# Performance work log

Hardware: AMD Instinct MI355X
Metric: run time of the kernel (lower is better)

Reference implementation:

```python
import jax, jax.numpy as jnp
import numpy as np


def _gru(x, h0, Wi, Wh, bi, bh):
    """PyTorch-equations GRU. x: (T,B,D), Wi: (3H,D), Wh: (3H,H). Returns (ys, hT)."""
    xW = jnp.einsum('tbd,gd->tbg', x, Wi) + bi  # (T,B,3H) precomputed input proj
    def step(h, xw):
        hw = h @ Wh.T + bh
        xr, xz, xn = jnp.split(xw, 3, axis=-1)
        hr, hz, hn = jnp.split(hw, 3, axis=-1)
        r = jax.nn.sigmoid(xr + hr)
        z = jax.nn.sigmoid(xz + hz)
        n = jnp.tanh(xn + r * hn)
        h_new = (1.0 - z) * n + z * h
        return h_new, h_new
    hT, ys = jax.lax.scan(step, h0, xW)
    return ys, hT


def _bigru(x, WiF, WhF, biF, bhF, WiB, WhB, biB, bhB):
    B = x.shape[1]
    H = WhF.shape[1]
    h0 = jnp.zeros((B, H), x.dtype)
    yf, hf = _gru(x, h0, WiF, WhF, biF, bhF)
    yb, hb = _gru(x[::-1], h0, WiB, WhB, biB, bhB)
    return jnp.concatenate([yf, yb[::-1]], axis=-1), jnp.stack([hf, hb], axis=0)


def _ln(x, g, b, eps=1e-5):
    mu = x.mean(-1, keepdims=True)
    var = ((x - mu) ** 2).mean(-1, keepdims=True)
    return (x - mu) * jax.lax.rsqrt(var + eps) * g + b


def _forward(tokens, emb,
             s_WiF, s_WhF, s_biF, s_bhF, s_lnF_g, s_lnF_b,
             s_Wi_f, s_Wh_f, s_bi_f, s_bh_f, s_Wi_b, s_Wh_b, s_bi_b, s_bh_b,
             s_ln_g, s_ln_b, s_linW, s_linb,
             d_WiF, d_WhF, d_biF, d_bhF, d_lnF_g, d_lnF_b,
             d_Wi_f, d_Wh_f, d_bi_f, d_bh_f, d_Wi_b, d_Wh_b, d_bi_b, d_bh_b,
             d_ln_g, d_ln_b, out_W, out_b):
    S, T, B = tokens.shape
    H = s_WhF.shape[1]
    # sentence loop is batch-independent -> fold sentences into batch
    x = emb[tokens]                                  # (S,T,B,E)
    x = x.transpose(1, 0, 2, 3).reshape(T, S * B, -1)  # (T, S*B, E)
    h0 = jnp.zeros((S * B, H), x.dtype)
    y, _ = _gru(x, h0, s_WiF, s_WhF, s_biF, s_bhF)
    y = _ln(y, s_lnF_g, s_lnF_b)
    y, _ = _bigru(y, s_Wi_f, s_Wh_f, s_bi_f, s_bh_f, s_Wi_b, s_Wh_b, s_bi_b, s_bh_b)
    y = _ln(y, s_ln_g, s_ln_b)
    y = jnp.tanh(y @ s_linW.T + s_linb)              # (T, S*B, H)
    store = y.mean(axis=0).reshape(S, B, H)          # per-sentence mean-pooled cell
    # document-level encoder over sentence sequence
    h0d = jnp.zeros((B, H), x.dtype)
    y, _ = _gru(store, h0d, d_WiF, d_WhF, d_biF, d_bhF)
    y = _ln(y, d_lnF_g, d_lnF_b)
    y, _ = _bigru(y, d_Wi_f, d_Wh_f, d_bi_f, d_bh_f, d_Wi_b, d_Wh_b, d_bi_b, d_bh_b)
    y = _ln(y, d_ln_g, d_ln_b)
    return jax.nn.sigmoid(y @ out_W.T + out_b)       # (S, B, O)


def setup_inputs() -> dict:
    V, E, H, O = 32000, 256, 256, 2
    S, T, B = 96, 32, 32
    keys = iter(jax.random.split(jax.random.key(0), 64))
    def g(shape, scale=0.06):
        return jax.random.normal(next(keys), shape, jnp.float32) * scale
    inp = {}
    inp['tokens'] = jax.random.randint(next(keys), (S, T, B), 0, V)
    inp['emb'] = g((V, E), 0.1)
    # sentence encoder: uni GRU (E->H), LN(H), bi GRU (H->H), LN(2H), linear 2H->H
    inp['s_WiF'] = g((3 * H, E)); inp['s_WhF'] = g((3 * H, H))
    inp['s_biF'] = jnp.zeros((3 * H,)); inp['s_bhF'] = jnp.zeros((3 * H,))
    inp['s_lnF_g'] = jnp.ones((H,)); inp['s_lnF_b'] = jnp.zeros((H,))
    inp['s_Wi_f'] = g((3 * H, H)); inp['s_Wh_f'] = g((3 * H, H))
    inp['s_bi_f'] = jnp.zeros((3 * H,)); inp['s_bh_f'] = jnp.zeros((3 * H,))
    inp['s_Wi_b'] = g((3 * H, H)); inp['s_Wh_b'] = g((3 * H, H))
    inp['s_bi_b'] = jnp.zeros((3 * H,)); inp['s_bh_b'] = jnp.zeros((3 * H,))
    inp['s_ln_g'] = jnp.ones((2 * H,)); inp['s_ln_b'] = jnp.zeros((2 * H,))
    inp['s_linW'] = g((H, 2 * H)); inp['s_linb'] = jnp.zeros((H,))
    # document encoder: uni GRU (H->H), LN(H), bi GRU (H->H), LN(2H)
    inp['d_WiF'] = g((3 * H, H)); inp['d_WhF'] = g((3 * H, H))
    inp['d_biF'] = jnp.zeros((3 * H,)); inp['d_bhF'] = jnp.zeros((3 * H,))
    inp['d_lnF_g'] = jnp.ones((H,)); inp['d_lnF_b'] = jnp.zeros((H,))
    inp['d_Wi_f'] = g((3 * H, H)); inp['d_Wh_f'] = g((3 * H, H))
    inp['d_bi_f'] = jnp.zeros((3 * H,)); inp['d_bh_f'] = jnp.zeros((3 * H,))
    inp['d_Wi_b'] = g((3 * H, H)); inp['d_Wh_b'] = g((3 * H, H))
    inp['d_bi_b'] = jnp.zeros((3 * H,)); inp['d_bh_b'] = jnp.zeros((3 * H,))
    inp['d_ln_g'] = jnp.ones((2 * H,)); inp['d_ln_b'] = jnp.zeros((2 * H,))
    inp['out_W'] = g((O, 2 * H)); inp['out_b'] = jnp.zeros((O,))
    return inp


def reference(tokens, emb,
              s_WiF, s_WhF, s_biF, s_bhF, s_lnF_g, s_lnF_b,
              s_Wi_f, s_Wh_f, s_bi_f, s_bh_f, s_Wi_b, s_Wh_b, s_bi_b, s_bh_b,
              s_ln_g, s_ln_b, s_linW, s_linb,
              d_WiF, d_WhF, d_biF, d_bhF, d_lnF_g, d_lnF_b,
              d_Wi_f, d_Wh_f, d_bi_f, d_bh_f, d_Wi_b, d_Wh_b, d_bi_b, d_bh_b,
              d_ln_g, d_ln_b, out_W, out_b):
    return _forward(tokens, emb,
                    s_WiF, s_WhF, s_biF, s_bhF, s_lnF_g, s_lnF_b,
                    s_Wi_f, s_Wh_f, s_bi_f, s_bh_f, s_Wi_b, s_Wh_b, s_bi_b, s_bh_b,
                    s_ln_g, s_ln_b, s_linW, s_linb,
                    d_WiF, d_WhF, d_biF, d_bhF, d_lnF_g, d_lnF_b,
                    d_Wi_f, d_Wh_f, d_bi_f, d_bh_f, d_Wi_b, d_Wh_b, d_bi_b, d_bh_b,
                    d_ln_g, d_ln_b, out_W, out_b)
```

## Files before the change

kernel.cpp:

```cpp
#include <hip/hip_runtime.h>


typedef __bf16 bf16;
typedef __bf16 bf16x8 __attribute__((ext_vector_type(8)));
typedef __bf16 bf16x4 __attribute__((ext_vector_type(4)));
typedef float  f32x4  __attribute__((ext_vector_type(4)));

static __device__ __forceinline__ f32x4 mfma16(bf16x8 a, bf16x8 b, f32x4 c) {
  return __builtin_amdgcn_mfma_f32_16x16x32_bf16(a, b, c, 0, 0, 0);
}
static __device__ __forceinline__ float sigm(float x) { return 1.f / (1.f + __expf(-x)); }
static __device__ __forceinline__ bf16x8 asbf(f32x4 v) {
  union { f32x4 f; bf16x8 b; } u; u.f = v; return u.b;
}
static __device__ __forceinline__ void wg_barrier() {
  asm volatile("s_waitcnt lgkmcnt(0)" ::: "memory");
  __builtin_amdgcn_s_barrier();
  __builtin_amdgcn_sched_barrier(0);
}
static __device__ __forceinline__ void gload16(const bf16* g, bf16* l) {
  __builtin_amdgcn_global_load_lds(
      (const __attribute__((address_space(1))) void*)g,
      (__attribute__((address_space(3))) void*)l, 16, 0, 0);
}

__global__ __launch_bounds__(256) void cvt_bf16(
    const float* __restrict__ s, bf16* __restrict__ d, int n4)
{
  int i = blockIdx.x * 256 + threadIdx.x;
  if (i < n4) {
    float4 v = ((const float4*)s)[i];
    bf16x4 o;
    o[0] = (bf16)v.x; o[1] = (bf16)v.y; o[2] = (bf16)v.z; o[3] = (bf16)v.w;
    ((bf16x4*)d)[i] = o;
  }
}

__global__ __launch_bounds__(256) void conv13(
    const float* s0, const float* s1, const float* s2, const float* s3,
    const float* s4, const float* s5, const float* s6, const float* s7,
    const float* s8, const float* s9, const float* s10, const float* s11,
    const float* s12, bf16* __restrict__ dst)
{
  const float* srcs[13] = {s0,s1,s2,s3,s4,s5,s6,s7,s8,s9,s10,s11,s12};
  int m = blockIdx.y;
  int n4 = (m == 12) ? 32768 : 49152;
  int i = blockIdx.x * 256 + threadIdx.x;
  if (i >= n4) return;
  float4 v = ((const float4*)srcs[m])[i];
  bf16x4 o;
  o[0] = (bf16)v.x; o[1] = (bf16)v.y; o[2] = (bf16)v.z; o[3] = (bf16)v.w;
  ((bf16x4*)(dst + (size_t)m * 196608))[i] = o;
}

__global__ __launch_bounds__(256) void prep_bias(
    const float* b0i, const float* b0h, const float* b1i, const float* b1h,
    const float* b2i, const float* b2h, const float* b3i, const float* b3h,
    const float* b4i, const float* b4h, const float* b5i, const float* b5h,
    float* __restrict__ out)
{
  const float* bis[6] = {b0i,b1i,b2i,b3i,b4i,b5i};
  const float* bhs[6] = {b0h,b1h,b2h,b3h,b4h,b5h};
  int g = blockIdx.y;
  int i = blockIdx.x * 256 + threadIdx.x;
  if (i < 768)
    out[g * 768 + i] = bis[g][i] + (i < 512 ? bhs[g][i] : 0.f);
}

__global__ __launch_bounds__(256) void xw_gemm(
    const bf16* __restrict__ X,
    const bf16* __restrict__ W0, const float* __restrict__ b0, bf16* __restrict__ o0,
    const bf16* __restrict__ W1, const float* __restrict__ b1, bf16* __restrict__ o1)
{
  const bf16* W = blockIdx.y ? W1 : W0;
  const float* bias = blockIdx.y ? b1 : b0;
  bf16* out = blockIdx.y ? o1 : o0;
  int wave = (int)blockIdx.x * 4 + (threadIdx.x >> 6);
  int g64 = wave / 48, ct = wave - g64 * 48;
  int lane = threadIdx.x & 63;
  int r16 = lane & 15, g4 = lane >> 4;
  const bf16* wp = W + (size_t)(ct * 16 + r16) * 256;
  const bf16* xb = X + ((size_t)g64 * 64 + r16) * 256;
  f32x4 a0 = {0,0,0,0}, a1 = {0,0,0,0}, a2 = {0,0,0,0}, a3 = {0,0,0,0};
#pragma unroll
  for (int kk = 0; kk < 8; kk++) {
    int k0 = kk * 32 + g4 * 8;
    bf16x8 wf = *(const bf16x8*)(wp + k0);
    a0 = mfma16(*(const bf16x8*)(xb + k0), wf, a0);
    a1 = mfma16(*(const bf16x8*)(xb + 4096 + k0), wf, a1);
    a2 = mfma16(*(const bf16x8*)(xb + 8192 + k0), wf, a2);
    a3 = mfma16(*(const bf16x8*)(xb + 12288 + k0), wf, a3);
  }
  float bv = bias[ct * 16 + r16];
#pragma unroll
  for (int rt = 0; rt < 4; rt++) {
    f32x4 ac = rt == 0 ? a0 : rt == 1 ? a1 : rt == 2 ? a2 : a3;
#pragma unroll
    for (int j = 0; j < 4; j++)
      out[(size_t)(g64 * 64 + rt * 16 + g4 * 4 + j) * 768 + ct * 16 + r16] = (bf16)(ac[j] + bv);
  }
}

__global__ __launch_bounds__(256) void xw_gather_gemm(
    const int* __restrict__ tok, const bf16* __restrict__ embb,
    const bf16* __restrict__ W, const float* __restrict__ bias,
    bf16* __restrict__ out, int c)
{
  int t = blockIdx.y;
  int wave = (int)blockIdx.x * 4 + (threadIdx.x >> 6);
  int g64 = wave / 48, ct = wave - g64 * 48;
  int lane = threadIdx.x & 63;
  int r16 = lane & 15, g4 = lane >> 4;
  const bf16* wp = W + (size_t)(ct * 16 + r16) * 256;
  const bf16* ap[4];
#pragma unroll
  for (int rt = 0; rt < 4; rt++) {
    int n = g64 * 64 + rt * 16 + r16;
    int tk = tok[((n >> 5) << 10) + (t << 5) + (n & 31)];
    ap[rt] = embb + (size_t)tk * 256;
  }
  f32x4 a0 = {0,0,0,0}, a1 = {0,0,0,0}, a2 = {0,0,0,0}, a3 = {0,0,0,0};
#pragma unroll
  for (int kk = 0; kk < 8; kk++) {
    int k0 = kk * 32 + g4 * 8;
    bf16x8 wf = *(const bf16x8*)(wp + k0);
    a0 = mfma16(*(const bf16x8*)(ap[0] + k0), wf, a0);
    a1 = mfma16(*(const bf16x8*)(ap[1] + k0), wf, a1);
    a2 = mfma16(*(const bf16x8*)(ap[2] + k0), wf, a2);
    a3 = mfma16(*(const bf16x8*)(ap[3] + k0), wf, a3);
  }
  float bv = bias[ct * 16 + r16];
#pragma unroll
  for (int rt = 0; rt < 4; rt++) {
    f32x4 ac = rt == 0 ? a0 : rt == 1 ? a1 : rt == 2 ? a2 : a3;
#pragma unroll
    for (int j = 0; j < 4; j++)
      out[((size_t)t * c + g64 * 64 + rt * 16 + g4 * 4 + j) * 768 + ct * 16 + r16] = (bf16)(ac[j] + bv);
  }
}

__global__ __launch_bounds__(512)
__attribute__((amdgpu_waves_per_eu(1, 2)))
void pgru(
    const bf16* __restrict__ xw0, const bf16* __restrict__ Wh0, const float* __restrict__ bh0,
    const bf16* __restrict__ xw1, const bf16* __restrict__ Wh1, const float* __restrict__ bh1,
    bf16* __restrict__ yout0, bf16* __restrict__ yout1, int ostride,
    const float* __restrict__ lng, const float* __restrict__ lnb,
    int steps, int Mtot, int rev0, int rev1)
{
  int dir = blockIdx.y;
  const bf16*  xw = dir ? xw1 : xw0;
  const bf16*  Wh = dir ? Wh1 : Wh0;
  const float* bh = dir ? bh1 : bh0;
  bf16* yout = dir ? yout1 : yout0;
  int rev = dir ? rev1 : rev0;

  __shared__ __align__(16) bf16 hbuf[16][280];
  __shared__ __align__(16) bf16 xbuf[3][8][3][16][32];

  int tid = threadIdx.x;
  int w = tid >> 6, lane = tid & 63, r16 = lane & 15, g4 = lane >> 4;
  int rowbase = (int)blockIdx.x * 16;
  int c0 = w * 32 + r16, c1 = c0 + 16;

  for (int i2 = tid; i2 < 560; i2 += 512) ((bf16x8*)hbuf)[i2] = (bf16x8){};

  f32x4 wr0[8], wz0[8], wn0[8], wr1[8], wz1[8], wn1[8];
  {
    const bf16* W0 = Wh + (size_t)c0 * 256;
    const bf16* W1 = Wh + (size_t)c1 * 256;
#pragma unroll
    for (int kk = 0; kk < 8; kk++) {
      int k0 = kk * 32 + g4 * 8;
      wr0[kk] = *(const f32x4*)(W0 + k0);          asm volatile("" : "+v"(wr0[kk]));
      wz0[kk] = *(const f32x4*)(W0 + 65536 + k0);  asm volatile("" : "+v"(wz0[kk]));
      wn0[kk] = *(const f32x4*)(W0 + 131072 + k0); asm volatile("" : "+v"(wn0[kk]));
      wr1[kk] = *(const f32x4*)(W1 + k0);          asm volatile("" : "+v"(wr1[kk]));
      wz1[kk] = *(const f32x4*)(W1 + 65536 + k0);  asm volatile("" : "+v"(wz1[kk]));
      wn1[kk] = *(const f32x4*)(W1 + 131072 + k0); asm volatile("" : "+v"(wn1[kk]));
    }
  }
  float bhn0 = bh[c0 + 512], bhn1 = bh[c1 + 512];

  int m_ = lane >> 2;
  int k_ = (lane & 3) * 8;
  auto stage = [&](int b, int st) {
    const bf16* s = xw + ((size_t)st * Mtot + rowbase + m_) * 768 + w * 32 + k_;
    gload16(s,       &xbuf[b][w][0][0][0]);
    gload16(s + 256, &xbuf[b][w][1][0][0]);
    gload16(s + 512, &xbuf[b][w][2][0][0]);
  };
  stage(0, rev ? steps - 1 : 0);
  wg_barrier();

  for (int i = 0; i < steps; i++) {
    int cur = i % 3;
    int st = rev ? steps - 1 - i : i;
    if (i + 1 < steps) {
      stage((i + 1) % 3, rev ? steps - 2 - i : i + 1);
      asm volatile("s_waitcnt vmcnt(3)" ::: "memory");
    } else {
      asm volatile("s_waitcnt vmcnt(0)" ::: "memory");
    }
    __builtin_amdgcn_sched_barrier(0);

    float hn0[4], hn1[4];
    {
      f32x4 a0 = {0,0,0,0}, a1 = {0,0,0,0}, a2 = {0,0,0,0};
#pragma unroll
      for (int kk = 0; kk < 8; kk++) {
        bf16x8 a = *(const bf16x8*)&hbuf[r16][kk * 32 + g4 * 8];
        a0 = mfma16(a, asbf(wr0[kk]), a0);
        a1 = mfma16(a, asbf(wz0[kk]), a1);
        a2 = mfma16(a, asbf(wn0[kk]), a2);
      }
#pragma unroll
      for (int j = 0; j < 4; j++) {
        int m = g4 * 4 + j;
        float r = sigm((float)xbuf[cur][w][0][m][r16] + a0[j]);
        float z = sigm((float)xbuf[cur][w][1][m][r16] + a1[j]);
        float n = tanhf((float)xbuf[cur][w][2][m][r16] + r * (a2[j] + bhn0));
        hn0[j] = (1.f - z) * n + z * (float)hbuf[m][c0];
      }
    }
    {
      f32x4 a0 = {0,0,0,0}, a1 = {0,0,0,0}, a2 = {0,0,0,0};
#pragma unroll
      for (int kk = 0; kk < 8; kk++) {
        bf16x8 a = *(const bf16x8*)&hbuf[r16][kk * 32 + g4 * 8];
        a0 = mfma16(a, asbf(wr1[kk]), a0);
        a1 = mfma16(a, asbf(wz1[kk]), a1);
        a2 = mfma16(a, asbf(wn1[kk]), a2);
      }
#pragma unroll
      for (int j = 0; j < 4; j++) {
        int m = g4 * 4 + j;
        float r = sigm((float)xbuf[cur][w][0][m][r16 + 16] + a0[j]);
        float z = sigm((float)xbuf[cur][w][1][m][r16 + 16] + a1[j]);
        float n = tanhf((float)xbuf[cur][w][2][m][r16 + 16] + r * (a2[j] + bhn1));
        hn1[j] = (1.f - z) * n + z * (float)hbuf[m][c1];
      }
    }
    wg_barrier();
#pragma unroll
    for (int j = 0; j < 4; j++) {
      int m = g4 * 4 + j;
      hbuf[m][c0] = (bf16)hn0[j];
      hbuf[m][c1] = (bf16)hn1[j];
    }
    if (!lng) {
#pragma unroll
      for (int j = 0; j < 4; j++) {
        size_t ro = ((size_t)st * Mtot + rowbase + g4 * 4 + j) * ostride;
        yout[ro + c0] = (bf16)hn0[j];
        yout[ro + c1] = (bf16)hn1[j];
      }
    }
    wg_barrier();
    if (lng) {
#pragma unroll
      for (int rr = 0; rr < 2; rr++) {
        int r = w * 2 + rr;
        bf16x4 v4 = *(const bf16x4*)&hbuf[r][lane * 4];
        float v[4]; float sm = 0.f, sq = 0.f;
#pragma unroll
        for (int j = 0; j < 4; j++) { v[j] = (float)v4[j]; sm += v[j]; sq += v[j] * v[j]; }
        for (int msk = 32; msk; msk >>= 1) { sm += __shfl_xor(sm, msk); sq += __shfl_xor(sq, msk); }
        float mu  = sm * (1.f / 256.f);
        float var = sq * (1.f / 256.f) - mu * mu;
        float inv = rsqrtf(fmaxf(var, 0.f) + 1e-5f);
        bf16x4 o;
#pragma unroll
        for (int j = 0; j < 4; j++)
          o[j] = (bf16)((v[j] - mu) * inv * lng[lane * 4 + j] + lnb[lane * 4 + j]);
        *(bf16x4*)&yout[((size_t)st * Mtot + rowbase + r) * ostride + lane * 4] = o;
      }
    }
  }
}

__global__ __launch_bounds__(256) void sent_tail_part(
    const bf16* __restrict__ hf, const bf16* __restrict__ hb,
    const float* __restrict__ gam, const float* __restrict__ bet,
    const bf16* __restrict__ W, const float* __restrict__ bias,
    float* __restrict__ part, int c)
{
  int wave = threadIdx.x >> 6;
  int lane = threadIdx.x & 63;
  int r16 = lane & 15, g4 = lane >> 4;
  int r0 = (int)blockIdx.x << 4;
  int tg = blockIdx.y;
  size_t rowoff = (size_t)(r0 + r16) * 256;

  f32x4 ms0 = {0,0,0,0}, ms1 = {0,0,0,0}, ms2 = {0,0,0,0}, ms3 = {0,0,0,0};

  for (int tt = 0; tt < 4; tt++) {
    int t = tg * 4 + tt;
    const bf16* pf = hf + (size_t)t * c * 256 + rowoff;
    const bf16* pb = hb + (size_t)t * c * 256 + rowoff;
    bf16x8 xv[16];
    float s = 0.f, sq = 0.f;
#pragma unroll
    for (int kk = 0; kk < 16; kk++) {
      int k0 = kk * 32 + g4 * 8;
      xv[kk] = (kk < 8) ? *(const bf16x8*)(pf + k0) : *(const bf16x8*)(pb + k0 - 256);
#pragma unroll
      for (int j = 0; j < 8; j++) { float f = (float)xv[kk][j]; s += f; sq += f * f; }
    }
    s  += __shfl_xor(s, 16);  s  += __shfl_xor(s, 32);
    sq += __shfl_xor(sq, 16); sq += __shfl_xor(sq, 32);
    float mu  = s * (1.f / 512.f);
    float var = sq * (1.f / 512.f) - mu * mu;
    float inv = rsqrtf(fmaxf(var, 0.f) + 1e-5f);
#pragma unroll
    for (int kk = 0; kk < 16; kk++) {
      int k0 = kk * 32 + g4 * 8;
      float ga[8], be[8];
      *(float4*)(ga)     = *(const float4*)(gam + k0);
      *(float4*)(ga + 4) = *(const float4*)(gam + k0 + 4);
      *(float4*)(be)     = *(const float4*)(bet + k0);
      *(float4*)(be + 4) = *(const float4*)(bet + k0 + 4);
#pragma unroll
      for (int j = 0; j < 8; j++)
        xv[kk][j] = (bf16)(((float)xv[kk][j] - mu) * inv * ga[j] + be[j]);
    }
#pragma unroll
    for (int tc = 0; tc < 4; tc++) {
      int cj = wave * 64 + tc * 16;
      const bf16* wp = W + (size_t)(cj + r16) * 512;
      f32x4 acc = {0,0,0,0};
#pragma unroll
      for (int kk = 0; kk < 16; kk++)
        acc = mfma16(xv[kk], *(const bf16x8*)(wp + kk * 32 + g4 * 8), acc);
      float bb = bias[cj + r16];
      f32x4* msp = (tc == 0) ? &ms0 : (tc == 1) ? &ms1 : (tc == 2) ? &ms2 : &ms3;
#pragma unroll
      for (int j = 0; j < 4; j++) (*msp)[j] += tanhf(acc[j] + bb);
    }
  }
#pragma unroll
  for (int tc = 0; tc < 4; tc++) {
    int cj = wave * 64 + tc * 16;
    f32x4 ms = (tc == 0) ? ms0 : (tc == 1) ? ms1 : (tc == 2) ? ms2 : ms3;
#pragma unroll
    for (int j = 0; j < 4; j++)
      part[((size_t)tg * c + r0 + g4 * 4 + j) * 256 + cj + r16] = ms[j];
  }
}

__global__ __launch_bounds__(256) void tail_reduce(
    const float* __restrict__ part, bf16* __restrict__ out, int c)
{
  int idx = blockIdx.x * 256 + threadIdx.x;
  float s = 0.f;
#pragma unroll
  for (int g = 0; g < 8; g++) s += part[(size_t)g * c * 256 + idx];
  out[idx] = (bf16)(s * 0.03125f);
}

__global__ __launch_bounds__(256) void ln_out_head(
    const bf16* __restrict__ X, const float* __restrict__ lng, const float* __restrict__ lnb,
    const float* __restrict__ W, const float* __restrict__ bias, float* __restrict__ out)
{
  int w = threadIdx.x >> 6, lane = threadIdx.x & 63;
  int row = (int)blockIdx.x * 4 + w;
  bf16x8 v8 = *(const bf16x8*)&X[(size_t)row * 512 + lane * 8];
  float v[8]; float sm = 0.f, sq = 0.f;
#pragma unroll
  for (int j = 0; j < 8; j++) { v[j] = (float)v8[j]; sm += v[j]; sq += v[j] * v[j]; }
  for (int msk = 32; msk; msk >>= 1) { sm += __shfl_xor(sm, msk); sq += __shfl_xor(sq, msk); }
  float mu  = sm * (1.f / 512.f);
  float var = sq * (1.f / 512.f) - mu * mu;
  float inv = rsqrtf(fmaxf(var, 0.f) + 1e-5f);
  float a0 = 0.f, a1 = 0.f;
  int base = lane * 8;
#pragma unroll
  for (int j = 0; j < 8; j++) {
    float y = (v[j] - mu) * inv * lng[base + j] + lnb[base + j];
    a0 += y * W[base + j];
    a1 += y * W[512 + base + j];
  }
  for (int msk = 32; msk; msk >>= 1) { a0 += __shfl_xor(a0, msk); a1 += __shfl_xor(a1, msk); }
  if (lane == 0) {
    out[(size_t)row * 2 + 0] = sigm(a0 + bias[0]);
    out[(size_t)row * 2 + 1] = sigm(a1 + bias[1]);
  }
}

extern "C" void kernel_launch(void* const* d_in, const int* in_sizes, int n_in,
                              void* d_out, int out_size, void* d_ws, size_t ws_size,
                              hipStream_t stream)
{
  (void)in_sizes; (void)n_in; (void)out_size;
  const int*   tokens = (const int*)d_in[0];
  const float* emb    = (const float*)d_in[1];
  auto fp = [&](int i) { return (const float*)d_in[i]; };
  const float *s_WiF = fp(2),  *s_WhF = fp(3),  *s_biF = fp(4),  *s_bhF = fp(5);
  const float *s_lnF_g = fp(6), *s_lnF_b = fp(7);
  const float *s_Wi_f = fp(8),  *s_Wh_f = fp(9),  *s_bi_f = fp(10), *s_bh_f = fp(11);
  const float *s_Wi_b = fp(12), *s_Wh_b = fp(13), *s_bi_b = fp(14), *s_bh_b = fp(15);
  const float *s_ln_g = fp(16), *s_ln_b = fp(17), *s_linW = fp(18), *s_linb = fp(19);
  const float *dWiF = fp(20), *dWhF = fp(21), *dbiF = fp(22), *dbhF = fp(23);
  const float *d_lnF_g = fp(24), *d_lnF_b = fp(25);
  const float *dWi_f = fp(26), *dWh_f = fp(27), *dbi_f = fp(28), *dbh_f = fp(29);
  const float *dWi_b = fp(30), *dWh_b = fp(31), *dbi_b = fp(32), *dbh_b = fp(33);
  const float *d_ln_g = fp(34), *d_ln_b = fp(35), *out_W = fp(36), *out_b = fp(37);

  const int T = 32, S = 96;
  const int GW = 196608;

  bf16* wc = (bf16*)d_ws;
  bf16 *c_sWiF = wc,         *c_sWhF = wc + GW;
  bf16 *c_sWif = wc + 2*GW,  *c_sWhf = wc + 3*GW;
  bf16 *c_sWib = wc + 4*GW,  *c_sWhb = wc + 5*GW;
  bf16 *c_dWiF = wc + 6*GW,  *c_dWhF = wc + 7*GW;
  bf16 *c_dWif = wc + 8*GW,  *c_dWhf = wc + 9*GW;
  bf16 *c_dWib = wc + 10*GW, *c_dWhb = wc + 11*GW;
  bf16 *c_linW = wc + 12*GW;
  const size_t WB = (size_t)(12 * GW + 131072) * 2;
  bf16* embb = (bf16*)((char*)d_ws + WB);
  const size_t EB = (size_t)32000 * 256 * 2;
  float* bmod = (float*)((char*)d_ws + WB + EB);
  const size_t BMB = 6 * 768 * 4;

  conv13<<<dim3(192, 13), 256, 0, stream>>>(
      s_WiF, s_WhF, s_Wi_f, s_Wh_f, s_Wi_b, s_Wh_b,
      dWiF, dWhF, dWi_f, dWh_f, dWi_b, dWh_b, s_linW, wc);
  cvt_bf16<<<8000, 256, 0, stream>>>(emb, embb, 2048000);
  prep_bias<<<dim3(3, 6), 256, 0, stream>>>(
      s_biF, s_bhF, s_bi_f, s_bh_f, s_bi_b, s_bh_b,
      dbiF, dbhF, dbi_f, dbh_f, dbi_b, dbh_b, bmod);
  const float *bm_sF = bmod, *bm_sf = bmod + 768, *bm_sb = bmod + 1536;
  const float *bm_dF = bmod + 2304, *bm_df = bmod + 3072, *bm_db = bmod + 3840;

  char* ws = (char*)d_ws + WB + EB + BMB;
  bf16* store = (bf16*)ws;
  bf16* yd1ln = store + (size_t)3072 * 256;
  bf16* ybid  = yd1ln + (size_t)3072 * 256;
  bf16* xw_u  = ybid  + (size_t)3072 * 512;
  bf16* xwdf  = xw_u  + (size_t)3072 * 768;
  bf16* xwdb  = xwdf  + (size_t)3072 * 768;
  const size_t fixedB = WB + EB + BMB
      + ((size_t)3072 * 256 * 2 + (size_t)3072 * 512 + (size_t)3 * 3072 * 768) * 2;

  int c = 3072;
  while (c > 192 && fixedB + (size_t)98304 * c > ws_size) c >>= 1;
  char* cb = (char*)d_ws + fixedB;
  bf16*  xw   = (bf16*)cb;
  bf16*  y1ln = (bf16*)(cb + (size_t)49152 * c);
  bf16*  hf   = (bf16*)(cb + (size_t)65536 * c);
  bf16*  hb   = (bf16*)(cb + (size_t)81920 * c);
  float* part = (float*)cb;

  for (int base = 0; base < 3072; base += c) {
    const int* tkb = tokens + (size_t)base * 32;
    xw_gather_gemm<<<dim3((c / 64) * 12, T), 256, 0, stream>>>(
        tkb, embb, c_sWiF, bm_sF, xw, c);
    pgru<<<dim3(c / 16, 1), 512, 0, stream>>>(
        xw, c_sWhF, s_bhF, nullptr, nullptr, nullptr,
        y1ln, nullptr, 256, s_lnF_g, s_lnF_b, T, c, 0, 0);
    xw_gemm<<<dim3((T * c / 64) * 12, 1), 256, 0, stream>>>(
        y1ln, c_sWif, bm_sf, xw, nullptr, nullptr, nullptr);
    pgru<<<dim3(c / 16, 1), 512, 0, stream>>>(
        xw, c_sWhf, s_bh_f, nullptr, nullptr, nullptr,
        hf, nullptr, 256, nullptr, nullptr, T, c, 0, 0);
    xw_gemm<<<dim3((T * c / 64) * 12, 1), 256, 0, stream>>>(
        y1ln, c_sWib, bm_sb, xw, nullptr, nullptr, nullptr);
    pgru<<<dim3(c / 16, 1), 512, 0, stream>>>(
        xw, c_sWhb, s_bh_b, nullptr, nullptr, nullptr,
        hb, nullptr, 256, nullptr, nullptr, T, c, 1, 0);
    sent_tail_part<<<dim3(c / 16, 8), 256, 0, stream>>>(
        hf, hb, s_ln_g, s_ln_b, c_linW, s_linb, part, c);
    tail_reduce<<<c, 256, 0, stream>>>(part, store + (size_t)base * 256, c);
  }

  xw_gemm<<<dim3((3072 / 64) * 12, 1), 256, 0, stream>>>(
      store, c_dWiF, bm_dF, xw_u, nullptr, nullptr, nullptr);
  pgru<<<dim3(2, 1), 512, 0, stream>>>(
      xw_u, c_dWhF, dbhF, nullptr, nullptr, nullptr,
      yd1ln, nullptr, 256, d_lnF_g, d_lnF_b, S, 32, 0, 0);
  xw_gemm<<<dim3((3072 / 64) * 12, 2), 256, 0, stream>>>(
      yd1ln, c_dWif, bm_df, xwdf, c_dWib, bm_db, xwdb);
  pgru<<<dim3(2, 2), 512, 0, stream>>>(
      xwdf, c_dWhf, dbh_f, xwdb, c_dWhb, dbh_b,
      ybid, ybid + 256, 512, nullptr, nullptr, S, 32, 0, 1);
  ln_out_head<<<768, 256, 0, stream>>>(ybid, d_ln_g, d_ln_b, out_W, out_b,
                                       (float*)d_out);
}
```

Before: 3.586 ms.

## Replace persistent sentence GRU kernels with per-timestep launches plus separate LayerNorm

The three sentence-level GRU passes no longer use the persistent pgru kernel that loops over time. Each timestep is now its own hstep launch, where a wave computes a 64x16 output tile with MFMA, reloading its slice of Wh and reading the previous hidden state from global memory. The fused LayerNorm moves into a separate ln_rows pass over the first layer's output. This trades in-kernel recurrence for kernel-launch boundaries as the step synchronisation, so it pays launch overhead, weight reloads and global-memory round trips on every step in exchange for spreading each step across more blocks.

```diff
diff --git a/kernel.cpp b/kernel.cpp
--- a/kernel.cpp
+++ b/kernel.cpp
@@ -137,6 +137,79 @@
     for (int j = 0; j < 4; j++)
       out[((size_t)t * c + g64 * 64 + rt * 16 + g4 * 4 + j) * 768 + ct * 16 + r16] = (bf16)(ac[j] + bv);
   }
+}
+
+__global__ __launch_bounds__(256) void hstep(
+    const bf16* __restrict__ xw, const bf16* __restrict__ hp,
+    bf16* __restrict__ ho, const bf16* __restrict__ Wh,
+    const float* __restrict__ bh, int M)
+{
+  int wave = (int)blockIdx.x * 4 + (threadIdx.x >> 6);
+  int rg = wave >> 4, ct = wave & 15;
+  int lane = threadIdx.x & 63;
+  int r16 = lane & 15, g4 = lane >> 4;
+  int c = ct * 16 + r16;
+
+  const bf16* wp = Wh + (size_t)c * 256;
+  bf16x8 wr[8], wz[8], wn[8];
+#pragma unroll
+  for (int kk = 0; kk < 8; kk++) {
+    int k0 = kk * 32 + g4 * 8;
+    wr[kk] = *(const bf16x8*)(wp + k0);
+    wz[kk] = *(const bf16x8*)(wp + 65536 + k0);
+    wn[kk] = *(const bf16x8*)(wp + 131072 + k0);
+  }
+  float bhn = bh[c + 512];
+
+#pragma unroll
+  for (int rt = 0; rt < 4; rt++) {
+    int rowb = rg * 64 + rt * 16;
+    f32x4 aR = {0,0,0,0}, aZ = {0,0,0,0}, aN = {0,0,0,0};
+    if (hp) {
+      const bf16* ha = hp + (size_t)(rowb + r16) * 256;
+#pragma unroll
+      for (int kk = 0; kk < 8; kk++) {
+        bf16x8 a = *(const bf16x8*)(ha + kk * 32 + g4 * 8);
+        aR = mfma16(a, wr[kk], aR);
+        aZ = mfma16(a, wz[kk], aZ);
+        aN = mfma16(a, wn[kk], aN);
+      }
+    }
+#pragma unroll
+    for (int j = 0; j < 4; j++) {
+      int row = rowb + g4 * 4 + j;
+      const bf16* xq = xw + (size_t)row * 768 + c;
+      float r = sigm((float)xq[0]   + aR[j]);
+      float z = sigm((float)xq[256] + aZ[j]);
+      float n = tanhf((float)xq[512] + r * (aN[j] + bhn));
+      float hpv = hp ? (float)hp[(size_t)row * 256 + c] : 0.f;
+      ho[(size_t)row * 256 + c] = (bf16)((1.f - z) * n + z * hpv);
+    }
+  }
+  (void)M;
+}
+
+__global__ __launch_bounds__(256) void ln_rows(
+    bf16* __restrict__ data, const float* __restrict__ gam, const float* __restrict__ bet,
+    int rows)
+{
+  int wid = threadIdx.x >> 6, lane = threadIdx.x & 63;
+  int row = (blockIdx.x << 2) + wid;
+  if (row >= rows) return;
+  bf16* p = data + (size_t)row * 256;
+  bf16x4 t4 = *(const bf16x4*)(p + lane * 4);
+  float v[4]; float s = 0.f, sq = 0.f;
+#pragma unroll
+  for (int j = 0; j < 4; j++) { v[j] = (float)t4[j]; s += v[j]; sq += v[j] * v[j]; }
+  for (int m = 32; m; m >>= 1) { s += __shfl_xor(s, m); sq += __shfl_xor(sq, m); }
+  float mu  = s * (1.f / 256.f);
+  float var = sq * (1.f / 256.f) - mu * mu;
+  float inv = rsqrtf(fmaxf(var, 0.f) + 1e-5f);
+  bf16x4 o;
+#pragma unroll
+  for (int j = 0; j < 4; j++)
+    o[j] = (bf16)((v[j] - mu) * inv * gam[lane * 4 + j] + bet[lane * 4 + j]);
+  *(bf16x4*)(p + lane * 4) = o;
 }
 
 __global__ __launch_bounds__(512)
@@ -446,29 +519,38 @@
   int c = 3072;
   while (c > 192 && fixedB + (size_t)98304 * c > ws_size) c >>= 1;
   char* cb = (char*)d_ws + fixedB;
-  bf16*  xw   = (bf16*)cb;
-  bf16*  y1ln = (bf16*)(cb + (size_t)49152 * c);
-  bf16*  hf   = (bf16*)(cb + (size_t)65536 * c);
-  bf16*  hb   = (bf16*)(cb + (size_t)81920 * c);
+  bf16*  xw = (bf16*)cb;
+  bf16*  y1 = (bf16*)(cb + (size_t)49152 * c);
+  bf16*  hf = (bf16*)(cb + (size_t)65536 * c);
+  bf16*  hb = (bf16*)(cb + (size_t)81920 * c);
   float* part = (float*)cb;
+
+  const size_t cH = (size_t)c * 256;
+  const size_t cX = (size_t)c * 768;
 
   for (int base = 0; base < 3072; base += c) {
     const int* tkb = tokens + (size_t)base * 32;
     xw_gather_gemm<<<dim3((c / 64) * 12, T), 256, 0, stream>>>(
         tkb, embb, c_sWiF, bm_sF, xw, c);
-    pgru<<<dim3(c / 16, 1), 512, 0, stream>>>(
-        xw, c_sWhF, s_bhF, nullptr, nullptr, nullptr,
-        y1ln, nullptr, 256, s_lnF_g, s_lnF_b, T, c, 0, 0);
+    for (int t = 0; t < T; t++)
+      hstep<<<c / 16, 256, 0, stream>>>(
+          xw + (size_t)t * cX, t ? y1 + (size_t)(t - 1) * cH : nullptr,
+          y1 + (size_t)t * cH, c_sWhF, s_bhF, c);
+    ln_rows<<<(T * c) / 4, 256, 0, stream>>>(y1, s_lnF_g, s_lnF_b, T * c);
     xw_gemm<<<dim3((T * c / 64) * 12, 1), 256, 0, stream>>>(
-        y1ln, c_sWif, bm_sf, xw, nullptr, nullptr, nullptr);
-    pgru<<<dim3(c / 16, 1), 512, 0, stream>>>(
-        xw, c_sWhf, s_bh_f, nullptr, nullptr, nullptr,
-        hf, nullptr, 256, nullptr, nullptr, T, c, 0, 0);
+        y1, c_sWif, bm_sf, xw, nullptr, nullptr, nullptr);
+    for (int i = 0; i < T; i++)
+      hstep<<<c / 16, 256, 0, stream>>>(
+          xw + (size_t)i * cX, i ? hf + (size_t)(i - 1) * cH : nullptr,
+          hf + (size_t)i * cH, c_sWhf, s_bh_f, c);
     xw_gemm<<<dim3((T * c / 64) * 12, 1), 256, 0, stream>>>(
-        y1ln, c_sWib, bm_sb, xw, nullptr, nullptr, nullptr);
-    pgru<<<dim3(c / 16, 1), 512, 0, stream>>>(
-        xw, c_sWhb, s_bh_b, nullptr, nullptr, nullptr,
-        hb, nullptr, 256, nullptr, nullptr, T, c, 1, 0);
+        y1, c_sWib, bm_sb, xw, nullptr, nullptr, nullptr);
+    for (int i = 0; i < T; i++) {
+      int tb = T - 1 - i;
+      hstep<<<c / 16, 256, 0, stream>>>(
+          xw + (size_t)tb * cX, i ? hb + (size_t)(tb + 1) * cH : nullptr,
+          hb + (size_t)tb * cH, c_sWhb, s_bh_b, c);
+    }
     sent_tail_part<<<dim3(c / 16, 8), 256, 0, stream>>>(
         hf, hb, s_ln_g, s_ln_b, c_linW, s_linb, part, c);
     tail_reduce<<<c, 256, 0, stream>>>(part, store + (size_t)base * 256, c);
```

Measured after the change: 6.154 ms. 71.6% more time.
